# Optimization experiments

Hardware: AMD Instinct MI355X
Metric: run time of the kernel (lower is better)

Reference implementation:

```python
import jax, jax.numpy as jnp
import numpy as np

EPS = 1e-5

def _layernorm(x, g, b):
    m = jnp.mean(x, axis=-1, keepdims=True)
    v = jnp.mean((x - m) ** 2, axis=-1, keepdims=True)
    return (x - m) * jax.lax.rsqrt(v + EPS) * g + b

def setup_inputs() -> dict:
    key = jax.random.key(0)
    ks = jax.random.split(key, 16)
    B, N, L, E, D, NL = 1, 40962, 256, 4, 163848, 6
    inp = {}
    inp['mesh_latent'] = jax.random.normal(ks[0], (B, N, L), dtype=jnp.float32)
    inp['edge_index'] = jax.random.randint(ks[1], (2, D), 0, N, dtype=jnp.int32)
    inp['edge_attr'] = jax.random.normal(ks[2], (D, E), dtype=jnp.float32)
    s_e = 1.0 / np.sqrt(2 * L + E)
    s_n = 1.0 / np.sqrt(2 * L)
    s_o = 1.0 / np.sqrt(L)
    inp['We_w'] = jax.random.uniform(ks[3], (NL, 2 * L + E, L), jnp.float32, -s_e, s_e)
    inp['We_b'] = jax.random.uniform(ks[4], (NL, L), jnp.float32, -s_e, s_e)
    inp['ln1_g'] = jnp.ones((NL, L), jnp.float32)
    inp['ln1_b'] = jnp.zeros((NL, L), jnp.float32)
    inp['Wn1_w'] = jax.random.uniform(ks[5], (NL, 2 * L, L), jnp.float32, -s_n, s_n)
    inp['Wn1_b'] = jax.random.uniform(ks[6], (NL, L), jnp.float32, -s_n, s_n)
    inp['ln2_g'] = jnp.ones((NL, L), jnp.float32)
    inp['ln2_b'] = jnp.zeros((NL, L), jnp.float32)
    inp['Wn2_w'] = jax.random.uniform(ks[7], (NL, L, L), jnp.float32, -s_o, s_o)
    inp['Wn2_b'] = jax.random.uniform(ks[8], (NL, L), jnp.float32, -s_o, s_o)
    return inp

def reference(mesh_latent, edge_index, edge_attr, We_w, We_b, ln1_g, ln1_b,
              Wn1_w, Wn1_b, ln2_g, ln2_b, Wn2_w, Wn2_b):
    src = edge_index[0]  # x_j (source)
    dst = edge_index[1]  # x_i (target), also aggregation index
    N = mesh_latent.shape[1]
    L = mesh_latent.shape[2]
    # precompute edge_attr contribution is layer-dependent, done inside scan

    def layer(x, p):
        we_w, we_b, g1, b1, wn1_w, wn1_b, g2, b2, wn2_w, wn2_b = p
        x_i = x[dst]  # [E, L] target node feats
        x_j = x[src]  # [E, L] source node feats
        # edge MLP on cat([x_i, x_j, edge_attr]) without materializing the concat
        h = x_i @ we_w[:L] + x_j @ we_w[L:2 * L] + edge_attr @ we_w[2 * L:] + we_b
        msg = jax.nn.silu(_layernorm(h, g1, b1))  # [E, L]
        agg = jax.ops.segment_sum(msg, dst, num_segments=N)  # [N, L]
        u = x @ wn1_w[:L] + agg @ wn1_w[L:] + wn1_b
        u = jax.nn.silu(_layernorm(u, g2, b2)) @ wn2_w + wn2_b
        return x + u, None

    params = (We_w, We_b, ln1_g, ln1_b, Wn1_w, Wn1_b, ln2_g, ln2_b, Wn2_w, Wn2_b)

    def per_sample(x):
        x_out, _ = jax.lax.scan(layer, x, params)
        return x_out

    return jax.vmap(per_sample)(mesh_latent)
```

## Files before the change

### kernel.cpp

```cpp
#include <hip/hip_runtime.h>
#include <hip/hip_bf16.h>
#include <math.h>


#define NNODES 40962
#define NEDGES 163848
#define NLAYERS 6

typedef __attribute__((ext_vector_type(8))) short short8;
typedef __attribute__((ext_vector_type(4))) float f32x4;

__device__ __forceinline__ void async_copy16(void* lds, const void* g) {
    __builtin_amdgcn_global_load_lds(
        (const __attribute__((address_space(1))) unsigned int*)g,
        (__attribute__((address_space(3))) unsigned int*)lds, 16, 0, 0);
}

__global__ __launch_bounds__(256) void wprep_kernel(
    const float* __restrict__ src, unsigned short* __restrict__ dst,
    int R, int C, size_t src_lstride, size_t src_hstride, int halves)
{
    __shared__ float t[32][33];
    const int b = blockIdx.z;
    src += (size_t)(b / halves) * src_lstride + (size_t)(b % halves) * src_hstride;
    dst += (size_t)b * R * C;
    const int tx = threadIdx.x & 31, ty = threadIdx.x >> 5;
    const int c0 = blockIdx.x * 32, r0 = blockIdx.y * 32;
    #pragma unroll
    for (int i = 0; i < 4; ++i)
        t[ty + 8 * i][tx] = src[(size_t)(r0 + ty + 8 * i) * C + c0 + tx];
    __syncthreads();
    #pragma unroll
    for (int i = 0; i < 4; ++i) {
        unsigned int u = __float_as_uint(t[tx][ty + 8 * i]);
        unsigned short h = (unsigned short)((u + 0x7FFFu + ((u >> 16) & 1u)) >> 16);
        dst[(size_t)(c0 + ty + 8 * i) * R + r0 + tx] = h;
    }
}

__global__ __launch_bounds__(256) void gemm_mfma(
    const float* __restrict__ A1, const float* __restrict__ A2,
    const unsigned short* __restrict__ BT,
    const float* __restrict__ bias, const float* __restrict__ resid,
    float* __restrict__ C, int M, int K, int ldC)
{
    __shared__ __align__(16) short Ah[128 * 40];
    __shared__ __align__(16) short Al[128 * 40];
    __shared__ __align__(16) short Bs[128 * 32];

    const int tid = threadIdx.x;
    const int wave = tid >> 6;
    const int lane = tid & 63;
    const int m0 = blockIdx.x * 128;
    const int n0 = blockIdx.y * 128;
    const int wm = wave >> 1;
    const int wn = wave & 1;
    const int fm = lane & 15;
    const int quad = lane >> 4;
    const int ko = quad * 8;

    const int arow = tid >> 1;
    const int akh = (tid & 1) * 16;
    const int gr_stage = m0 + arow;

    f32x4 acc[4][4];
    #pragma unroll
    for (int i = 0; i < 4; ++i)
        #pragma unroll
        for (int j = 0; j < 4; ++j)
            acc[i][j] = (f32x4){0.f, 0.f, 0.f, 0.f};

    const int nkt = K >> 5;
    for (int kt = 0; kt < nkt; ++kt) {
        const int k0 = kt << 5;
        const float* Asrc; int kb;
        if (A2 != nullptr && k0 >= 256) { Asrc = A2; kb = k0 - 256; }
        else                            { Asrc = A1; kb = k0; }

        {
            const int n_row = wave * 32 + (lane >> 2);
            const char* gbase = (const char*)BT + (((size_t)(n0 + n_row) * K + k0) << 1)
                              + ((lane & 3) << 4);
            char* lbase = (char*)Bs + wave * 2048;
            async_copy16(lbase, gbase);
            const char* gbase2 = gbase + ((size_t)16 * K << 1);
            async_copy16(lbase + 1024, gbase2);
        }

        {
            float f[16];
            if (gr_stage < M) {
                const float* ap = Asrc + (size_t)gr_stage * 256 + kb + akh;
                #pragma unroll
                for (int i = 0; i < 4; ++i) {
                    f32x4 v = *(const f32x4*)(ap + 4 * i);
                    f[4 * i + 0] = v.x; f[4 * i + 1] = v.y;
                    f[4 * i + 2] = v.z; f[4 * i + 3] = v.w;
                }
            } else {
                #pragma unroll
                for (int i = 0; i < 16; ++i) f[i] = 0.f;
            }
            unsigned int hid[8], lod[8];
            #pragma unroll
            for (int i = 0; i < 8; ++i) {
                unsigned int u0 = __float_as_uint(f[2 * i]);
                unsigned int u1 = __float_as_uint(f[2 * i + 1]);
                float l0 = f[2 * i]     - __uint_as_float(u0 & 0xFFFF0000u);
                float l1 = f[2 * i + 1] - __uint_as_float(u1 & 0xFFFF0000u);
                hid[i] = (u0 >> 16) | (u1 & 0xFFFF0000u);
                lod[i] = (__float_as_uint(l0) >> 16) | (__float_as_uint(l1) & 0xFFFF0000u);
            }
            short* ah = &Ah[arow * 40 + akh];
            short* al = &Al[arow * 40 + akh];
            ((uint4*)ah)[0] = make_uint4(hid[0], hid[1], hid[2], hid[3]);
            ((uint4*)ah)[1] = make_uint4(hid[4], hid[5], hid[6], hid[7]);
            ((uint4*)al)[0] = make_uint4(lod[0], lod[1], lod[2], lod[3]);
            ((uint4*)al)[1] = make_uint4(lod[4], lod[5], lod[6], lod[7]);
        }

        __syncthreads();

        short8 afh[4], afl[4], bf[4];
        #pragma unroll
        for (int i = 0; i < 4; ++i) {
            const int r = wm * 64 + i * 16 + fm;
            afh[i] = *(const short8*)&Ah[r * 40 + ko];
            afl[i] = *(const short8*)&Al[r * 40 + ko];
        }
        #pragma unroll
        for (int j = 0; j < 4; ++j) {
            const int r = wn * 64 + j * 16 + fm;
            bf[j] = *(const short8*)&Bs[r * 32 + ko];
        }
        #pragma unroll
        for (int i = 0; i < 4; ++i)
            #pragma unroll
            for (int j = 0; j < 4; ++j) {
                acc[i][j] = __builtin_amdgcn_mfma_f32_16x16x32_bf16(afl[i], bf[j], acc[i][j], 0, 0, 0);
                acc[i][j] = __builtin_amdgcn_mfma_f32_16x16x32_bf16(afh[i], bf[j], acc[i][j], 0, 0, 0);
            }

        __syncthreads();
    }

    #pragma unroll
    for (int j = 0; j < 4; ++j) {
        const int gc = n0 + wn * 64 + j * 16 + fm;
        const float bj = bias ? bias[gc] : 0.f;
        #pragma unroll
        for (int i = 0; i < 4; ++i) {
            #pragma unroll
            for (int r = 0; r < 4; ++r) {
                const int gr = m0 + wm * 64 + i * 16 + quad * 4 + r;
                if (gr < M) {
                    float v = acc[i][j][r] + bj;
                    if (resid) v += resid[(size_t)gr * ldC + gc];
                    C[(size_t)gr * ldC + gc] = v;
                }
            }
        }
    }
}

__device__ __forceinline__ float wave_sum(float v) {
    #pragma unroll
    for (int o = 32; o > 0; o >>= 1) v += __shfl_xor(v, o);
    return v;
}

__global__ __launch_bounds__(256) void count_kernel(
    const int* __restrict__ dst, int* __restrict__ deg, int E)
{
    int e = blockIdx.x * 256 + threadIdx.x;
    if (e < E) atomicAdd(&deg[dst[e]], 1);
}

__global__ __launch_bounds__(1024) void scan_kernel(
    const int* __restrict__ deg, int* __restrict__ rowptr, int n)
{
    __shared__ int wsum[16];
    __shared__ int carry_s;
    const int tid = threadIdx.x;
    const int lane = tid & 63, wave = tid >> 6;
    if (tid == 0) carry_s = 0;
    __syncthreads();

    for (int base = 0; base < n; base += 1024) {
        int i = base + tid;
        int v = (i < n) ? deg[i] : 0;
        int x = v;
        #pragma unroll
        for (int o = 1; o < 64; o <<= 1) {
            int t = __shfl_up(x, o);
            if (lane >= o) x += t;
        }
        if (lane == 63) wsum[wave] = x;
        __syncthreads();
        if (wave == 0 && lane < 16) {
            int w = wsum[lane];
            #pragma unroll
            for (int o = 1; o < 16; o <<= 1) {
                int t = __shfl_up(w, o);
                if (lane >= o) w += t;
            }
            wsum[lane] = w;
        }
        __syncthreads();
        int wave_off = (wave == 0) ? 0 : wsum[wave - 1];
        int incl = x + wave_off + carry_s;
        if (i < n) rowptr[i] = incl - v;
        __syncthreads();
        if (tid == 0) carry_s += wsum[15];
        __syncthreads();
    }
    if (tid == 0) rowptr[n] = carry_s;
}

__global__ __launch_bounds__(256) void scatter_kernel(
    const int* __restrict__ dst, int* __restrict__ cursor,
    int* __restrict__ esorted, int E)
{
    int e = blockIdx.x * 256 + threadIdx.x;
    if (e < E) {
        int p = atomicAdd(&cursor[dst[e]], 1);
        esorted[p] = e;
    }
}

__global__ __launch_bounds__(256) void node_agg_kernel(
    const float* __restrict__ P,
    const int* __restrict__ src,
    const float* __restrict__ attr,
    const float* __restrict__ W3,
    const float* __restrict__ be, const float* __restrict__ g1, const float* __restrict__ b1,
    const int* __restrict__ rowptr, const int* __restrict__ esorted,
    float* __restrict__ agg, int N)
{
    const int wave = threadIdx.x >> 6;
    const int lane = threadIdx.x & 63;
    const int n = blockIdx.x * 4 + wave;
    if (n >= N) return;
    const int c0 = lane * 4;

    float4 p1 = *(const float4*)(P + (size_t)n * 512 + c0);
    const float* p1p = (const float*)&p1;

    float w30[4], w31[4], w32[4], w33[4], bev[4], g1v[4], b1v[4];
    #pragma unroll
    for (int i = 0; i < 4; ++i) {
        const int c = c0 + i;
        w30[i] = W3[c]; w31[i] = W3[256 + c]; w32[i] = W3[512 + c]; w33[i] = W3[768 + c];
        bev[i] = be[c]; g1v[i] = g1[c]; b1v[i] = b1[c];
    }

    float acc[4] = {0.f, 0.f, 0.f, 0.f};
    const int beg = rowptr[n];
    const int end = rowptr[n + 1];

    for (int i = beg; i < end; ++i) {
        const int e = esorted[i];
        const int s = src[e];
        float4 ps = *(const float4*)(P + (size_t)s * 512 + 256 + c0);
        const float* psp = (const float*)&ps;
        float4 av = *(const float4*)(attr + (size_t)e * 4);

        float h[4];
        #pragma unroll
        for (int j = 0; j < 4; ++j) {
            float w = av.x * w30[j] + av.y * w31[j] + av.z * w32[j] + av.w * w33[j];
            h[j] = p1p[j] + psp[j] + w + bev[j];
        }

        float sum = wave_sum(h[0] + h[1] + h[2] + h[3]);
        const float mean = sum * (1.0f / 256.0f);
        float vs = 0.f;
        #pragma unroll
        for (int j = 0; j < 4; ++j) { float t = h[j] - mean; vs += t * t; }
        vs = wave_sum(vs);
        const float rstd = rsqrtf(vs * (1.0f / 256.0f) + 1e-5f);

        #pragma unroll
        for (int j = 0; j < 4; ++j) {
            float y = (h[j] - mean) * rstd * g1v[j] + b1v[j];
            acc[j] += y / (1.0f + __expf(-y));
        }
    }

    *(float4*)(agg + (size_t)n * 256 + c0) = make_float4(acc[0], acc[1], acc[2], acc[3]);
}

__global__ __launch_bounds__(256) void ln_silu_kernel(
    float* __restrict__ u, const float* __restrict__ g, const float* __restrict__ b, int N)
{
    const int wave = threadIdx.x >> 6;
    const int lane = threadIdx.x & 63;
    const int r = blockIdx.x * 4 + wave;
    if (r >= N) return;

    float4 hv = *(const float4*)(u + (size_t)r * 256 + lane * 4);
    float h[4] = {hv.x, hv.y, hv.z, hv.w};

    float sum = wave_sum(h[0] + h[1] + h[2] + h[3]);
    const float mean = sum * (1.0f / 256.0f);
    float vs = 0.f;
    #pragma unroll
    for (int i = 0; i < 4; ++i) { float t = h[i] - mean; vs += t * t; }
    vs = wave_sum(vs);
    const float rstd = rsqrtf(vs * (1.0f / 256.0f) + 1e-5f);

    #pragma unroll
    for (int i = 0; i < 4; ++i) {
        const int c = lane * 4 + i;
        float y = (h[i] - mean) * rstd * g[c] + b[c];
        h[i] = y / (1.0f + __expf(-y));
    }
    *(float4*)(u + (size_t)r * 256 + lane * 4) = make_float4(h[0], h[1], h[2], h[3]);
}

extern "C" void kernel_launch(void* const* d_in, const int* in_sizes, int n_in,
                              void* d_out, int out_size, void* d_ws, size_t ws_size,
                              hipStream_t stream) {
    const float* mesh   = (const float*)d_in[0];
    const int*   eidx   = (const int*)  d_in[1];
    const float* eattr  = (const float*)d_in[2];
    const float* We_w   = (const float*)d_in[3];
    const float* We_b   = (const float*)d_in[4];
    const float* ln1_g  = (const float*)d_in[5];
    const float* ln1_b  = (const float*)d_in[6];
    const float* Wn1_w  = (const float*)d_in[7];
    const float* Wn1_b  = (const float*)d_in[8];
    const float* ln2_g  = (const float*)d_in[9];
    const float* ln2_b  = (const float*)d_in[10];
    const float* Wn2_w  = (const float*)d_in[11];
    const float* Wn2_b  = (const float*)d_in[12];

    const int N = NNODES, E = NEDGES;

    float* x   = (float*)d_out;
    float* P   = (float*)d_ws;
    float* u   = P;
    float* agg = P + (size_t)N * 512;
    int*   deg     = (int*)(agg + (size_t)N * 256);
    int*   rowptr  = deg + N;
    int*   cursor  = rowptr + (N + 1);
    int*   esorted = cursor + N;
    uintptr_t wp = (uintptr_t)(esorted + E);
    wp = (wp + 63) & ~(uintptr_t)63;
    unsigned short* BTe  = (unsigned short*)wp;
    unsigned short* BTn1 = BTe  + (size_t)6 * 512 * 256;
    unsigned short* BTn2 = BTn1 + (size_t)6 * 256 * 512;

    const int* src = eidx;
    const int* dst = eidx + E;

    hipMemcpyAsync(x, mesh, (size_t)N * 256 * sizeof(float),
                   hipMemcpyDeviceToDevice, stream);

    wprep_kernel<<<dim3(8, 8, 12), 256, 0, stream>>>(
        We_w, BTe, 256, 256, (size_t)516 * 256, (size_t)256 * 256, 2);
    wprep_kernel<<<dim3(8, 16, 6), 256, 0, stream>>>(
        Wn1_w, BTn1, 512, 256, (size_t)512 * 256, 0, 1);
    wprep_kernel<<<dim3(8, 8, 6), 256, 0, stream>>>(
        Wn2_w, BTn2, 256, 256, (size_t)256 * 256, 0, 1);

    hipMemsetAsync(deg, 0, (size_t)N * sizeof(int), stream);
    count_kernel<<<(E + 255) / 256, 256, 0, stream>>>(dst, deg, E);
    scan_kernel<<<1, 1024, 0, stream>>>(deg, rowptr, N);
    hipMemcpyAsync(cursor, rowptr, (size_t)N * sizeof(int),
                   hipMemcpyDeviceToDevice, stream);
    scatter_kernel<<<(E + 255) / 256, 256, 0, stream>>>(dst, cursor, esorted, E);

    const int mblocks = (N + 127) / 128;
    const int node_blocks = (N + 3) / 4;

    for (int l = 0; l < NLAYERS; ++l) {
        const float* W3  = We_w + (size_t)l * 516 * 256 + (size_t)512 * 256;
        const float* be  = We_b  + (size_t)l * 256;
        const float* g1  = ln1_g + (size_t)l * 256;
        const float* b1  = ln1_b + (size_t)l * 256;
        const float* bn1 = Wn1_b + (size_t)l * 256;
        const float* g2  = ln2_g + (size_t)l * 256;
        const float* b2  = ln2_b + (size_t)l * 256;
        const float* bn2 = Wn2_b + (size_t)l * 256;
        const unsigned short* bte  = BTe  + (size_t)l * 512 * 256;
        const unsigned short* btn1 = BTn1 + (size_t)l * 256 * 512;
        const unsigned short* btn2 = BTn2 + (size_t)l * 256 * 256;

        gemm_mfma<<<dim3(mblocks, 4), 256, 0, stream>>>(
            x, nullptr, bte, nullptr, nullptr, P, N, 256, 512);
        node_agg_kernel<<<node_blocks, 256, 0, stream>>>(
            P, src, eattr, W3, be, g1, b1, rowptr, esorted, agg, N);
        gemm_mfma<<<dim3(mblocks, 2), 256, 0, stream>>>(
            x, agg, btn1, bn1, nullptr, u, N, 512, 256);
        ln_silu_kernel<<<node_blocks, 256, 0, stream>>>(u, g2, b2, N);
        gemm_mfma<<<dim3(mblocks, 2), 256, 0, stream>>>(
            u, nullptr, btn2, bn2, x, x, N, 256, 256);
    }
}
```

Baseline: 1.527 ms.

## Fuse node LayerNorm+SiLU into GEMM A-load and prefetch edges in aggregation

The ln_silu kernel is replaced by a stats-only kernel that writes per-row mean and rstd. The LayerNorm and SiLU are then applied while the third GEMM stages its A tile, which removes one full read-modify-write pass over u. The node aggregation loop now prefetches the next edge's gather and attribute loads, and it computes mean and variance in a single fused shuffle reduction (E[x^2]-mean^2). The single-pass variance is less numerically robust, and the GEMM load path gains extra per-element exp work.

```diff
diff --git a/kernel.cpp b/kernel.cpp
--- a/kernel.cpp
+++ b/kernel.cpp
@@ -42,6 +42,8 @@
     const float* __restrict__ A1, const float* __restrict__ A2,
     const unsigned short* __restrict__ BT,
     const float* __restrict__ bias, const float* __restrict__ resid,
+    const float2* __restrict__ lnstats, const float* __restrict__ lng,
+    const float* __restrict__ lnb,
     float* __restrict__ C, int M, int K, int ldC)
 {
     __shared__ __align__(16) short Ah[128 * 40];
@@ -96,6 +98,15 @@
                     f32x4 v = *(const f32x4*)(ap + 4 * i);
                     f[4 * i + 0] = v.x; f[4 * i + 1] = v.y;
                     f[4 * i + 2] = v.z; f[4 * i + 3] = v.w;
+                }
+                if (lnstats != nullptr) {
+                    const float2 st = lnstats[gr_stage];
+                    #pragma unroll
+                    for (int i = 0; i < 16; ++i) {
+                        const int c = k0 + akh + i;
+                        float y = (f[i] - st.x) * st.y * lng[c] + lnb[c];
+                        f[i] = y / (1.0f + __expf(-y));
+                    }
                 }
             } else {
                 #pragma unroll
@@ -258,27 +269,43 @@
     const int beg = rowptr[n];
     const int end = rowptr[n + 1];
 
+    float4 ps = make_float4(0.f, 0.f, 0.f, 0.f);
+    float4 av = make_float4(0.f, 0.f, 0.f, 0.f);
+    if (beg < end) {
+        const int e = esorted[beg];
+        const int s = src[e];
+        ps = *(const float4*)(P + (size_t)s * 512 + 256 + c0);
+        av = *(const float4*)(attr + (size_t)e * 4);
+    }
+
     for (int i = beg; i < end; ++i) {
-        const int e = esorted[i];
-        const int s = src[e];
-        float4 ps = *(const float4*)(P + (size_t)s * 512 + 256 + c0);
-        const float* psp = (const float*)&ps;
-        float4 av = *(const float4*)(attr + (size_t)e * 4);
-
+        const float4 ps_c = ps;
+        const float4 av_c = av;
+        if (i + 1 < end) {
+            const int e2 = esorted[i + 1];
+            const int s2 = src[e2];
+            ps = *(const float4*)(P + (size_t)s2 * 512 + 256 + c0);
+            av = *(const float4*)(attr + (size_t)e2 * 4);
+        }
+
+        const float* psp = (const float*)&ps_c;
         float h[4];
         #pragma unroll
         for (int j = 0; j < 4; ++j) {
-            float w = av.x * w30[j] + av.y * w31[j] + av.z * w32[j] + av.w * w33[j];
+            float w = av_c.x * w30[j] + av_c.y * w31[j] + av_c.z * w32[j] + av_c.w * w33[j];
             h[j] = p1p[j] + psp[j] + w + bev[j];
         }
 
-        float sum = wave_sum(h[0] + h[1] + h[2] + h[3]);
-        const float mean = sum * (1.0f / 256.0f);
-        float vs = 0.f;
-        #pragma unroll
-        for (int j = 0; j < 4; ++j) { float t = h[j] - mean; vs += t * t; }
-        vs = wave_sum(vs);
-        const float rstd = rsqrtf(vs * (1.0f / 256.0f) + 1e-5f);
+        float s_ = h[0] + h[1] + h[2] + h[3];
+        float q_ = h[0] * h[0] + h[1] * h[1] + h[2] * h[2] + h[3] * h[3];
+        #pragma unroll
+        for (int o = 32; o > 0; o >>= 1) {
+            s_ += __shfl_xor(s_, o);
+            q_ += __shfl_xor(q_, o);
+        }
+        const float mean = s_ * (1.0f / 256.0f);
+        const float var  = q_ * (1.0f / 256.0f) - mean * mean;
+        const float rstd = rsqrtf(var + 1e-5f);
 
         #pragma unroll
         for (int j = 0; j < 4; ++j) {
@@ -290,8 +317,8 @@
     *(float4*)(agg + (size_t)n * 256 + c0) = make_float4(acc[0], acc[1], acc[2], acc[3]);
 }
 
-__global__ __launch_bounds__(256) void ln_silu_kernel(
-    float* __restrict__ u, const float* __restrict__ g, const float* __restrict__ b, int N)
+__global__ __launch_bounds__(256) void row_stats_kernel(
+    const float* __restrict__ u, float2* __restrict__ stats, int N)
 {
     const int wave = threadIdx.x >> 6;
     const int lane = threadIdx.x & 63;
@@ -299,23 +326,18 @@
     if (r >= N) return;
 
     float4 hv = *(const float4*)(u + (size_t)r * 256 + lane * 4);
-    float h[4] = {hv.x, hv.y, hv.z, hv.w};
-
-    float sum = wave_sum(h[0] + h[1] + h[2] + h[3]);
-    const float mean = sum * (1.0f / 256.0f);
-    float vs = 0.f;
-    #pragma unroll
-    for (int i = 0; i < 4; ++i) { float t = h[i] - mean; vs += t * t; }
-    vs = wave_sum(vs);
-    const float rstd = rsqrtf(vs * (1.0f / 256.0f) + 1e-5f);
-
-    #pragma unroll
-    for (int i = 0; i < 4; ++i) {
-        const int c = lane * 4 + i;
-        float y = (h[i] - mean) * rstd * g[c] + b[c];
-        h[i] = y / (1.0f + __expf(-y));
-    }
-    *(float4*)(u + (size_t)r * 256 + lane * 4) = make_float4(h[0], h[1], h[2], h[3]);
+    float s_ = hv.x + hv.y + hv.z + hv.w;
+    float q_ = hv.x * hv.x + hv.y * hv.y + hv.z * hv.z + hv.w * hv.w;
+    #pragma unroll
+    for (int o = 32; o > 0; o >>= 1) {
+        s_ += __shfl_xor(s_, o);
+        q_ += __shfl_xor(q_, o);
+    }
+    if (lane == 0) {
+        const float mean = s_ * (1.0f / 256.0f);
+        const float var  = q_ * (1.0f / 256.0f) - mean * mean;
+        stats[r] = make_float2(mean, rsqrtf(var + 1e-5f));
+    }
 }
 
 extern "C" void kernel_launch(void* const* d_in, const int* in_sizes, int n_in,
@@ -350,6 +372,7 @@
     unsigned short* BTe  = (unsigned short*)wp;
     unsigned short* BTn1 = BTe  + (size_t)6 * 512 * 256;
     unsigned short* BTn2 = BTn1 + (size_t)6 * 256 * 512;
+    float2* stats = (float2*)(BTn2 + (size_t)6 * 256 * 256);
 
     const int* src = eidx;
     const int* dst = eidx + E;
@@ -388,13 +411,16 @@
         const unsigned short* btn2 = BTn2 + (size_t)l * 256 * 256;
 
         gemm_mfma<<<dim3(mblocks, 4), 256, 0, stream>>>(
-            x, nullptr, bte, nullptr, nullptr, P, N, 256, 512);
+            x, nullptr, bte, nullptr, nullptr, nullptr, nullptr, nullptr,
+            P, N, 256, 512);
         node_agg_kernel<<<node_blocks, 256, 0, stream>>>(
             P, src, eattr, W3, be, g1, b1, rowptr, esorted, agg, N);
         gemm_mfma<<<dim3(mblocks, 2), 256, 0, stream>>>(
-            x, agg, btn1, bn1, nullptr, u, N, 512, 256);
-        ln_silu_kernel<<<node_blocks, 256, 0, stream>>>(u, g2, b2, N);
+            x, agg, btn1, bn1, nullptr, nullptr, nullptr, nullptr,
+            u, N, 512, 256);
+        row_stats_kernel<<<node_blocks, 256, 0, stream>>>(u, stats, N);
         gemm_mfma<<<dim3(mblocks, 2), 256, 0, stream>>>(
-            u, nullptr, btn2, bn2, x, x, N, 256, 256);
-    }
-}
+            u, nullptr, btn2, bn2, x, stats, g2, b2,
+            x, N, 256, 256);
+    }
+}
```

After: 1.588 ms. 4.0% more time.

## Store activations pre-split into bf16 hi/lo planes and async-load GEMM A tiles

Applied to the files above, without the earlier changes.

Producers now write activations as separate bf16 high and low planes: the init copy, the node aggregation, the LN+SiLU kernel and the residual GEMM epilogue. The GEMM can then stage its A tiles straight into LDS with global_load_lds instead of loading fp32, splitting in registers and storing. This halves A-operand bytes per GEMM and removes the split ALU work from the inner loop. In exchange it adds extra hi/lo stores in the epilogues and drops the LDS padding, which may cause bank conflicts. The node aggregation kernel also processes two edges per wave using 32-lane halves with 8 columns each, and both layernorms switch to a single-pass sum and sum-of-squares variance.

```diff
diff --git a/kernel.cpp b/kernel.cpp
--- a/kernel.cpp
+++ b/kernel.cpp
@@ -14,6 +14,14 @@
     __builtin_amdgcn_global_load_lds(
         (const __attribute__((address_space(1))) unsigned int*)g,
         (__attribute__((address_space(3))) unsigned int*)lds, 16, 0, 0);
+}
+
+__device__ __forceinline__ void split2(float a, float b, unsigned int& hi, unsigned int& lo) {
+    unsigned int u0 = __float_as_uint(a), u1 = __float_as_uint(b);
+    float l0 = a - __uint_as_float(u0 & 0xFFFF0000u);
+    float l1 = b - __uint_as_float(u1 & 0xFFFF0000u);
+    hi = (u0 >> 16) | (u1 & 0xFFFF0000u);
+    lo = (__float_as_uint(l0) >> 16) | (__float_as_uint(l1) & 0xFFFF0000u);
 }
 
 __global__ __launch_bounds__(256) void wprep_kernel(
@@ -38,30 +46,41 @@
     }
 }
 
+__global__ __launch_bounds__(256) void init_split_kernel(
+    const float* __restrict__ mesh, float* __restrict__ x,
+    unsigned short* __restrict__ xh, unsigned short* __restrict__ xl, int total4)
+{
+    int i = blockIdx.x * 256 + threadIdx.x;
+    if (i >= total4) return;
+    f32x4 v = ((const f32x4*)mesh)[i];
+    ((f32x4*)x)[i] = v;
+    unsigned int h0, l0, h1, l1;
+    split2(v.x, v.y, h0, l0);
+    split2(v.z, v.w, h1, l1);
+    ((uint2*)xh)[i] = make_uint2(h0, h1);
+    ((uint2*)xl)[i] = make_uint2(l0, l1);
+}
+
 __global__ __launch_bounds__(256) void gemm_mfma(
-    const float* __restrict__ A1, const float* __restrict__ A2,
+    const unsigned short* __restrict__ A1h, const unsigned short* __restrict__ A1l,
+    const unsigned short* __restrict__ A2h, const unsigned short* __restrict__ A2l,
     const unsigned short* __restrict__ BT,
     const float* __restrict__ bias, const float* __restrict__ resid,
-    float* __restrict__ C, int M, int K, int ldC)
-{
-    __shared__ __align__(16) short Ah[128 * 40];
-    __shared__ __align__(16) short Al[128 * 40];
+    float* __restrict__ C, unsigned short* __restrict__ Ch, unsigned short* __restrict__ Cl,
+    int M, int K, int ldC)
+{
+    __shared__ __align__(16) short Ah[128 * 32];
+    __shared__ __align__(16) short Al[128 * 32];
     __shared__ __align__(16) short Bs[128 * 32];
 
     const int tid = threadIdx.x;
-    const int wave = tid >> 6;
-    const int lane = tid & 63;
-    const int m0 = blockIdx.x * 128;
-    const int n0 = blockIdx.y * 128;
-    const int wm = wave >> 1;
-    const int wn = wave & 1;
-    const int fm = lane & 15;
-    const int quad = lane >> 4;
-    const int ko = quad * 8;
-
-    const int arow = tid >> 1;
-    const int akh = (tid & 1) * 16;
-    const int gr_stage = m0 + arow;
+    const int wave = tid >> 6, lane = tid & 63;
+    const int m0 = blockIdx.x * 128, n0 = blockIdx.y * 128;
+    const int wm = wave >> 1, wn = wave & 1;
+    const int fm = lane & 15, quad = lane >> 4, ko = quad * 8;
+
+    const int r_in = lane >> 2;
+    const int seg  = lane & 3;
 
     f32x4 acc[4][4];
     #pragma unroll
@@ -73,50 +92,18 @@
     const int nkt = K >> 5;
     for (int kt = 0; kt < nkt; ++kt) {
         const int k0 = kt << 5;
-        const float* Asrc; int kb;
-        if (A2 != nullptr && k0 >= 256) { Asrc = A2; kb = k0 - 256; }
-        else                            { Asrc = A1; kb = k0; }
-
-        {
-            const int n_row = wave * 32 + (lane >> 2);
-            const char* gbase = (const char*)BT + (((size_t)(n0 + n_row) * K + k0) << 1)
-                              + ((lane & 3) << 4);
-            char* lbase = (char*)Bs + wave * 2048;
-            async_copy16(lbase, gbase);
-            const char* gbase2 = gbase + ((size_t)16 * K << 1);
-            async_copy16(lbase + 1024, gbase2);
-        }
-
-        {
-            float f[16];
-            if (gr_stage < M) {
-                const float* ap = Asrc + (size_t)gr_stage * 256 + kb + akh;
-                #pragma unroll
-                for (int i = 0; i < 4; ++i) {
-                    f32x4 v = *(const f32x4*)(ap + 4 * i);
-                    f[4 * i + 0] = v.x; f[4 * i + 1] = v.y;
-                    f[4 * i + 2] = v.z; f[4 * i + 3] = v.w;
-                }
-            } else {
-                #pragma unroll
-                for (int i = 0; i < 16; ++i) f[i] = 0.f;
-            }
-            unsigned int hid[8], lod[8];
-            #pragma unroll
-            for (int i = 0; i < 8; ++i) {
-                unsigned int u0 = __float_as_uint(f[2 * i]);
-                unsigned int u1 = __float_as_uint(f[2 * i + 1]);
-                float l0 = f[2 * i]     - __uint_as_float(u0 & 0xFFFF0000u);
-                float l1 = f[2 * i + 1] - __uint_as_float(u1 & 0xFFFF0000u);
-                hid[i] = (u0 >> 16) | (u1 & 0xFFFF0000u);
-                lod[i] = (__float_as_uint(l0) >> 16) | (__float_as_uint(l1) & 0xFFFF0000u);
-            }
-            short* ah = &Ah[arow * 40 + akh];
-            short* al = &Al[arow * 40 + akh];
-            ((uint4*)ah)[0] = make_uint4(hid[0], hid[1], hid[2], hid[3]);
-            ((uint4*)ah)[1] = make_uint4(hid[4], hid[5], hid[6], hid[7]);
-            ((uint4*)al)[0] = make_uint4(lod[0], lod[1], lod[2], lod[3]);
-            ((uint4*)al)[1] = make_uint4(lod[4], lod[5], lod[6], lod[7]);
+        const unsigned short *Ahs, *Als; int kb;
+        if (A2h != nullptr && k0 >= 256) { Ahs = A2h; Als = A2l; kb = k0 - 256; }
+        else                             { Ahs = A1h; Als = A1l; kb = k0; }
+
+        #pragma unroll
+        for (int i = 0; i < 2; ++i) {
+            const int r = wave * 32 + i * 16 + r_in;
+            int gr = m0 + r; if (gr > M - 1) gr = M - 1;
+            const int lbase = (wave * 32 + i * 16) * 32;
+            async_copy16(&Ah[lbase], Ahs + (size_t)gr * 256 + kb + seg * 8);
+            async_copy16(&Al[lbase], Als + (size_t)gr * 256 + kb + seg * 8);
+            async_copy16(&Bs[lbase], BT + (size_t)(n0 + r) * K + k0 + seg * 8);
         }
 
         __syncthreads();
@@ -125,8 +112,8 @@
         #pragma unroll
         for (int i = 0; i < 4; ++i) {
             const int r = wm * 64 + i * 16 + fm;
-            afh[i] = *(const short8*)&Ah[r * 40 + ko];
-            afl[i] = *(const short8*)&Al[r * 40 + ko];
+            afh[i] = *(const short8*)&Ah[r * 32 + ko];
+            afl[i] = *(const short8*)&Al[r * 32 + ko];
         }
         #pragma unroll
         for (int j = 0; j < 4; ++j) {
@@ -157,16 +144,16 @@
                     float v = acc[i][j][r] + bj;
                     if (resid) v += resid[(size_t)gr * ldC + gc];
                     C[(size_t)gr * ldC + gc] = v;
+                    if (Ch) {
+                        unsigned int u = __float_as_uint(v);
+                        float lo = v - __uint_as_float(u & 0xFFFF0000u);
+                        Ch[(size_t)gr * ldC + gc] = (unsigned short)(u >> 16);
+                        Cl[(size_t)gr * ldC + gc] = (unsigned short)(__float_as_uint(lo) >> 16);
+                    }
                 }
             }
         }
     }
-}
-
-__device__ __forceinline__ float wave_sum(float v) {
-    #pragma unroll
-    for (int o = 32; o > 0; o >>= 1) v += __shfl_xor(v, o);
-    return v;
 }
 
 __global__ __launch_bounds__(256) void count_kernel(
@@ -235,63 +222,97 @@
     const float* __restrict__ W3,
     const float* __restrict__ be, const float* __restrict__ g1, const float* __restrict__ b1,
     const int* __restrict__ rowptr, const int* __restrict__ esorted,
-    float* __restrict__ agg, int N)
+    unsigned short* __restrict__ aggh, unsigned short* __restrict__ aggl, int N)
 {
     const int wave = threadIdx.x >> 6;
     const int lane = threadIdx.x & 63;
+    const int half = lane >> 5;
+    const int l32  = lane & 31;
     const int n = blockIdx.x * 4 + wave;
     if (n >= N) return;
-    const int c0 = lane * 4;
-
-    float4 p1 = *(const float4*)(P + (size_t)n * 512 + c0);
-    const float* p1p = (const float*)&p1;
-
-    float w30[4], w31[4], w32[4], w33[4], bev[4], g1v[4], b1v[4];
-    #pragma unroll
-    for (int i = 0; i < 4; ++i) {
-        const int c = c0 + i;
-        w30[i] = W3[c]; w31[i] = W3[256 + c]; w32[i] = W3[512 + c]; w33[i] = W3[768 + c];
-        bev[i] = be[c]; g1v[i] = g1[c]; b1v[i] = b1[c];
-    }
-
-    float acc[4] = {0.f, 0.f, 0.f, 0.f};
+    const int c0 = l32 * 8;
+
+    float p1[8];
+    {
+        f32x4 a = *(const f32x4*)(P + (size_t)n * 512 + c0);
+        f32x4 b = *(const f32x4*)(P + (size_t)n * 512 + c0 + 4);
+        p1[0] = a.x; p1[1] = a.y; p1[2] = a.z; p1[3] = a.w;
+        p1[4] = b.x; p1[5] = b.y; p1[6] = b.z; p1[7] = b.w;
+    }
+
+    float w3v[4][8], bev[8], g1v[8], b1v[8];
+    #pragma unroll
+    for (int r = 0; r < 4; ++r) {
+        f32x4 a = *(const f32x4*)(W3 + r * 256 + c0);
+        f32x4 b = *(const f32x4*)(W3 + r * 256 + c0 + 4);
+        w3v[r][0] = a.x; w3v[r][1] = a.y; w3v[r][2] = a.z; w3v[r][3] = a.w;
+        w3v[r][4] = b.x; w3v[r][5] = b.y; w3v[r][6] = b.z; w3v[r][7] = b.w;
+    }
+    {
+        f32x4 a, b;
+        a = *(const f32x4*)(be + c0); b = *(const f32x4*)(be + c0 + 4);
+        bev[0]=a.x; bev[1]=a.y; bev[2]=a.z; bev[3]=a.w; bev[4]=b.x; bev[5]=b.y; bev[6]=b.z; bev[7]=b.w;
+        a = *(const f32x4*)(g1 + c0); b = *(const f32x4*)(g1 + c0 + 4);
+        g1v[0]=a.x; g1v[1]=a.y; g1v[2]=a.z; g1v[3]=a.w; g1v[4]=b.x; g1v[5]=b.y; g1v[6]=b.z; g1v[7]=b.w;
+        a = *(const f32x4*)(b1 + c0); b = *(const f32x4*)(b1 + c0 + 4);
+        b1v[0]=a.x; b1v[1]=a.y; b1v[2]=a.z; b1v[3]=a.w; b1v[4]=b.x; b1v[5]=b.y; b1v[6]=b.z; b1v[7]=b.w;
+    }
+
+    float acc[8] = {0.f, 0.f, 0.f, 0.f, 0.f, 0.f, 0.f, 0.f};
     const int beg = rowptr[n];
     const int end = rowptr[n + 1];
 
-    for (int i = beg; i < end; ++i) {
+    for (int i = beg + half; i < end; i += 2) {
         const int e = esorted[i];
         const int s = src[e];
-        float4 ps = *(const float4*)(P + (size_t)s * 512 + 256 + c0);
-        const float* psp = (const float*)&ps;
-        float4 av = *(const float4*)(attr + (size_t)e * 4);
-
-        float h[4];
-        #pragma unroll
-        for (int j = 0; j < 4; ++j) {
-            float w = av.x * w30[j] + av.y * w31[j] + av.z * w32[j] + av.w * w33[j];
-            h[j] = p1p[j] + psp[j] + w + bev[j];
-        }
-
-        float sum = wave_sum(h[0] + h[1] + h[2] + h[3]);
-        const float mean = sum * (1.0f / 256.0f);
-        float vs = 0.f;
-        #pragma unroll
-        for (int j = 0; j < 4; ++j) { float t = h[j] - mean; vs += t * t; }
-        vs = wave_sum(vs);
-        const float rstd = rsqrtf(vs * (1.0f / 256.0f) + 1e-5f);
-
-        #pragma unroll
-        for (int j = 0; j < 4; ++j) {
+        f32x4 pa = *(const f32x4*)(P + (size_t)s * 512 + 256 + c0);
+        f32x4 pb = *(const f32x4*)(P + (size_t)s * 512 + 256 + c0 + 4);
+        f32x4 av = *(const f32x4*)(attr + (size_t)e * 4);
+        float ps[8] = {pa.x, pa.y, pa.z, pa.w, pb.x, pb.y, pb.z, pb.w};
+
+        float h[8];
+        #pragma unroll
+        for (int j = 0; j < 8; ++j) {
+            float w = av.x * w3v[0][j] + av.y * w3v[1][j] + av.z * w3v[2][j] + av.w * w3v[3][j];
+            h[j] = p1[j] + ps[j] + w + bev[j];
+        }
+
+        float s_ = ((h[0] + h[1]) + (h[2] + h[3])) + ((h[4] + h[5]) + (h[6] + h[7]));
+        float q_ = ((h[0]*h[0] + h[1]*h[1]) + (h[2]*h[2] + h[3]*h[3]))
+                 + ((h[4]*h[4] + h[5]*h[5]) + (h[6]*h[6] + h[7]*h[7]));
+        #pragma unroll
+        for (int o = 16; o > 0; o >>= 1) {
+            s_ += __shfl_xor(s_, o);
+            q_ += __shfl_xor(q_, o);
+        }
+        const float mean = s_ * (1.0f / 256.0f);
+        const float var  = q_ * (1.0f / 256.0f) - mean * mean;
+        const float rstd = rsqrtf(var + 1e-5f);
+
+        #pragma unroll
+        for (int j = 0; j < 8; ++j) {
             float y = (h[j] - mean) * rstd * g1v[j] + b1v[j];
             acc[j] += y / (1.0f + __expf(-y));
         }
     }
 
-    *(float4*)(agg + (size_t)n * 256 + c0) = make_float4(acc[0], acc[1], acc[2], acc[3]);
-}
-
-__global__ __launch_bounds__(256) void ln_silu_kernel(
-    float* __restrict__ u, const float* __restrict__ g, const float* __restrict__ b, int N)
+    #pragma unroll
+    for (int j = 0; j < 8; ++j) acc[j] += __shfl_xor(acc[j], 32);
+
+    if (half == 0) {
+        unsigned int h0, l0, h1, l1, h2, l2, h3, l3;
+        split2(acc[0], acc[1], h0, l0);
+        split2(acc[2], acc[3], h1, l1);
+        split2(acc[4], acc[5], h2, l2);
+        split2(acc[6], acc[7], h3, l3);
+        *(uint4*)(aggh + (size_t)n * 256 + c0) = make_uint4(h0, h1, h2, h3);
+        *(uint4*)(aggl + (size_t)n * 256 + c0) = make_uint4(l0, l1, l2, l3);
+    }
+}
+
+__global__ __launch_bounds__(256) void ln_silu_split_kernel(
+    const float* __restrict__ u, const float* __restrict__ g, const float* __restrict__ b,
+    unsigned short* __restrict__ uh, unsigned short* __restrict__ ul, int N)
 {
     const int wave = threadIdx.x >> 6;
     const int lane = threadIdx.x & 63;
@@ -301,13 +322,16 @@
     float4 hv = *(const float4*)(u + (size_t)r * 256 + lane * 4);
     float h[4] = {hv.x, hv.y, hv.z, hv.w};
 
-    float sum = wave_sum(h[0] + h[1] + h[2] + h[3]);
-    const float mean = sum * (1.0f / 256.0f);
-    float vs = 0.f;
-    #pragma unroll
-    for (int i = 0; i < 4; ++i) { float t = h[i] - mean; vs += t * t; }
-    vs = wave_sum(vs);
-    const float rstd = rsqrtf(vs * (1.0f / 256.0f) + 1e-5f);
+    float s_ = (h[0] + h[1]) + (h[2] + h[3]);
+    float q_ = (h[0]*h[0] + h[1]*h[1]) + (h[2]*h[2] + h[3]*h[3]);
+    #pragma unroll
+    for (int o = 32; o > 0; o >>= 1) {
+        s_ += __shfl_xor(s_, o);
+        q_ += __shfl_xor(q_, o);
+    }
+    const float mean = s_ * (1.0f / 256.0f);
+    const float var  = q_ * (1.0f / 256.0f) - mean * mean;
+    const float rstd = rsqrtf(var + 1e-5f);
 
     #pragma unroll
     for (int i = 0; i < 4; ++i) {
@@ -315,7 +339,11 @@
         float y = (h[i] - mean) * rstd * g[c] + b[c];
         h[i] = y / (1.0f + __expf(-y));
     }
-    *(float4*)(u + (size_t)r * 256 + lane * 4) = make_float4(h[0], h[1], h[2], h[3]);
+    unsigned int h0, l0, h1, l1;
+    split2(h[0], h[1], h0, l0);
+    split2(h[2], h[3], h1, l1);
+    ((uint2*)(uh + (size_t)r * 256))[lane] = make_uint2(h0, h1);
+    ((uint2*)(ul + (size_t)r * 256))[lane] = make_uint2(l0, l1);
 }
 
 extern "C" void kernel_launch(void* const* d_in, const int* in_sizes, int n_in,
@@ -337,14 +365,21 @@
 
     const int N = NNODES, E = NEDGES;
 
-    float* x   = (float*)d_out;
-    float* P   = (float*)d_ws;
-    float* u   = P;
-    float* agg = P + (size_t)N * 512;
-    int*   deg     = (int*)(agg + (size_t)N * 256);
-    int*   rowptr  = deg + N;
-    int*   cursor  = rowptr + (N + 1);
-    int*   esorted = cursor + N;
+    float* x = (float*)d_out;
+
+    float* P = (float*)d_ws;
+    float* u = P;
+    unsigned short* uh = (unsigned short*)(P + (size_t)N * 256);
+    unsigned short* ul = uh + (size_t)N * 256;
+
+    unsigned short* xh   = (unsigned short*)(P + (size_t)N * 512);
+    unsigned short* xl   = xh + (size_t)N * 256;
+    unsigned short* aggh = xl + (size_t)N * 256;
+    unsigned short* aggl = aggh + (size_t)N * 256;
+    int* deg     = (int*)(aggl + (size_t)N * 256);
+    int* rowptr  = deg + N;
+    int* cursor  = rowptr + (N + 1);
+    int* esorted = cursor + N;
     uintptr_t wp = (uintptr_t)(esorted + E);
     wp = (wp + 63) & ~(uintptr_t)63;
     unsigned short* BTe  = (unsigned short*)wp;
@@ -354,8 +389,8 @@
     const int* src = eidx;
     const int* dst = eidx + E;
 
-    hipMemcpyAsync(x, mesh, (size_t)N * 256 * sizeof(float),
-                   hipMemcpyDeviceToDevice, stream);
+    const int total4 = N * 64;
+    init_split_kernel<<<(total4 + 255) / 256, 256, 0, stream>>>(mesh, x, xh, xl, total4);
 
     wprep_kernel<<<dim3(8, 8, 12), 256, 0, stream>>>(
         We_w, BTe, 256, 256, (size_t)516 * 256, (size_t)256 * 256, 2);
@@ -388,13 +423,16 @@
         const unsigned short* btn2 = BTn2 + (size_t)l * 256 * 256;
 
         gemm_mfma<<<dim3(mblocks, 4), 256, 0, stream>>>(
-            x, nullptr, bte, nullptr, nullptr, P, N, 256, 512);
+            xh, xl, nullptr, nullptr, bte, nullptr, nullptr,
+            P, nullptr, nullptr, N, 256, 512);
         node_agg_kernel<<<node_blocks, 256, 0, stream>>>(
-            P, src, eattr, W3, be, g1, b1, rowptr, esorted, agg, N);
+            P, src, eattr, W3, be, g1, b1, rowptr, esorted, aggh, aggl, N);
         gemm_mfma<<<dim3(mblocks, 2), 256, 0, stream>>>(
-            x, agg, btn1, bn1, nullptr, u, N, 512, 256);
-        ln_silu_kernel<<<node_blocks, 256, 0, stream>>>(u, g2, b2, N);
+            xh, xl, aggh, aggl, btn1, bn1, nullptr,
+            u, nullptr, nullptr, N, 512, 256);
+        ln_silu_split_kernel<<<node_blocks, 256, 0, stream>>>(u, g2, b2, uh, ul, N);
         gemm_mfma<<<dim3(mblocks, 2), 256, 0, stream>>>(
-            u, nullptr, btn2, bn2, x, x, N, 256, 256);
-    }
-}
+            uh, ul, nullptr, nullptr, btn2, bn2, x,
+            x, xh, xl, N, 256, 256);
+    }
+}
```

Result: slower. 1.738 ms (+13.8%).

## Drop LDS staging in GEMM and fuse LayerNorm+SiLU into Wn2 GEMM prologue

Applied to the files above, without the earlier changes.

The GEMM kernel no longer stages A and B tiles through shared memory with barriers. Each wave now loads its MFMA fragments straight from global memory and splits fp32 A into hi/lo bf16 in registers. The separate LN2+SiLU pass is replaced by a row-statistics kernel that writes only mean/rstd. The final GEMM applies normalization and SiLU to A on load, which saves a full read-modify-write of u. The cost is redundant global loads, since each A row is reloaded by both wn waves and each B row by both wm waves, with no coalesced LDS reuse; the SiLU is also recomputed per N-tile. The variance now uses E[x^2]-mean^2, which is less numerically stable.

```diff
diff --git a/kernel.cpp b/kernel.cpp
--- a/kernel.cpp
+++ b/kernel.cpp
@@ -10,10 +10,23 @@
 typedef __attribute__((ext_vector_type(8))) short short8;
 typedef __attribute__((ext_vector_type(4))) float f32x4;
 
-__device__ __forceinline__ void async_copy16(void* lds, const void* g) {
-    __builtin_amdgcn_global_load_lds(
-        (const __attribute__((address_space(1))) unsigned int*)g,
-        (__attribute__((address_space(3))) unsigned int*)lds, 16, 0, 0);
+union pack8 { uint4 u4; short8 s8; };
+
+__device__ __forceinline__ void split8(const float* f, short8& hi, short8& lo) {
+    unsigned int h[4], l[4];
+    #pragma unroll
+    for (int i = 0; i < 4; ++i) {
+        unsigned int u0 = __float_as_uint(f[2 * i]);
+        unsigned int u1 = __float_as_uint(f[2 * i + 1]);
+        float l0 = f[2 * i]     - __uint_as_float(u0 & 0xFFFF0000u);
+        float l1 = f[2 * i + 1] - __uint_as_float(u1 & 0xFFFF0000u);
+        h[i] = (u0 >> 16) | (u1 & 0xFFFF0000u);
+        l[i] = (__float_as_uint(l0) >> 16) | (__float_as_uint(l1) & 0xFFFF0000u);
+    }
+    pack8 ph, pl;
+    ph.u4 = make_uint4(h[0], h[1], h[2], h[3]);
+    pl.u4 = make_uint4(l[0], l[1], l[2], l[3]);
+    hi = ph.s8; lo = pl.s8;
 }
 
 __global__ __launch_bounds__(256) void wprep_kernel(
@@ -42,26 +55,28 @@
     const float* __restrict__ A1, const float* __restrict__ A2,
     const unsigned short* __restrict__ BT,
     const float* __restrict__ bias, const float* __restrict__ resid,
+    const float2* __restrict__ lnstats, const float* __restrict__ lng,
+    const float* __restrict__ lnb,
     float* __restrict__ C, int M, int K, int ldC)
 {
-    __shared__ __align__(16) short Ah[128 * 40];
-    __shared__ __align__(16) short Al[128 * 40];
-    __shared__ __align__(16) short Bs[128 * 32];
-
     const int tid = threadIdx.x;
-    const int wave = tid >> 6;
-    const int lane = tid & 63;
-    const int m0 = blockIdx.x * 128;
-    const int n0 = blockIdx.y * 128;
-    const int wm = wave >> 1;
-    const int wn = wave & 1;
-    const int fm = lane & 15;
-    const int quad = lane >> 4;
-    const int ko = quad * 8;
-
-    const int arow = tid >> 1;
-    const int akh = (tid & 1) * 16;
-    const int gr_stage = m0 + arow;
+    const int wave = tid >> 6, lane = tid & 63;
+    const int m0 = blockIdx.x * 128, n0 = blockIdx.y * 128;
+    const int wm = wave >> 1, wn = wave & 1;
+    const int fm = lane & 15, quad = lane >> 4, ko = quad * 8;
+
+    int arow[4];
+    float2 st[4];
+    #pragma unroll
+    for (int i = 0; i < 4; ++i) {
+        int r = m0 + wm * 64 + i * 16 + fm;
+        arow[i] = (r < M) ? r : (M - 1);
+        st[i] = lnstats ? lnstats[arow[i]] : make_float2(0.f, 0.f);
+    }
+    const unsigned short* brow[4];
+    #pragma unroll
+    for (int j = 0; j < 4; ++j)
+        brow[j] = BT + (size_t)(n0 + wn * 64 + j * 16 + fm) * K;
 
     f32x4 acc[4][4];
     #pragma unroll
@@ -77,62 +92,40 @@
         if (A2 != nullptr && k0 >= 256) { Asrc = A2; kb = k0 - 256; }
         else                            { Asrc = A1; kb = k0; }
 
-        {
-            const int n_row = wave * 32 + (lane >> 2);
-            const char* gbase = (const char*)BT + (((size_t)(n0 + n_row) * K + k0) << 1)
-                              + ((lane & 3) << 4);
-            char* lbase = (char*)Bs + wave * 2048;
-            async_copy16(lbase, gbase);
-            const char* gbase2 = gbase + ((size_t)16 * K << 1);
-            async_copy16(lbase + 1024, gbase2);
-        }
-
-        {
-            float f[16];
-            if (gr_stage < M) {
-                const float* ap = Asrc + (size_t)gr_stage * 256 + kb + akh;
+        short8 bf[4];
+        #pragma unroll
+        for (int j = 0; j < 4; ++j)
+            bf[j] = *(const short8*)(brow[j] + k0 + ko);
+
+        float gg[8], bb[8];
+        if (lnstats) {
+            f32x4 g0 = *(const f32x4*)(lng + k0 + ko);
+            f32x4 g1 = *(const f32x4*)(lng + k0 + ko + 4);
+            f32x4 b0 = *(const f32x4*)(lnb + k0 + ko);
+            f32x4 b1 = *(const f32x4*)(lnb + k0 + ko + 4);
+            gg[0]=g0.x; gg[1]=g0.y; gg[2]=g0.z; gg[3]=g0.w;
+            gg[4]=g1.x; gg[5]=g1.y; gg[6]=g1.z; gg[7]=g1.w;
+            bb[0]=b0.x; bb[1]=b0.y; bb[2]=b0.z; bb[3]=b0.w;
+            bb[4]=b1.x; bb[5]=b1.y; bb[6]=b1.z; bb[7]=b1.w;
+        }
+
+        short8 afh[4], afl[4];
+        #pragma unroll
+        for (int i = 0; i < 4; ++i) {
+            const float* ap = Asrc + (size_t)arow[i] * 256 + kb + ko;
+            f32x4 v0 = *(const f32x4*)ap;
+            f32x4 v1 = *(const f32x4*)(ap + 4);
+            float f[8] = {v0.x, v0.y, v0.z, v0.w, v1.x, v1.y, v1.z, v1.w};
+            if (lnstats) {
                 #pragma unroll
-                for (int i = 0; i < 4; ++i) {
-                    f32x4 v = *(const f32x4*)(ap + 4 * i);
-                    f[4 * i + 0] = v.x; f[4 * i + 1] = v.y;
-                    f[4 * i + 2] = v.z; f[4 * i + 3] = v.w;
+                for (int t = 0; t < 8; ++t) {
+                    float y = (f[t] - st[i].x) * st[i].y * gg[t] + bb[t];
+                    f[t] = y / (1.0f + __expf(-y));
                 }
-            } else {
-                #pragma unroll
-                for (int i = 0; i < 16; ++i) f[i] = 0.f;
             }
-            unsigned int hid[8], lod[8];
-            #pragma unroll
-            for (int i = 0; i < 8; ++i) {
-                unsigned int u0 = __float_as_uint(f[2 * i]);
-                unsigned int u1 = __float_as_uint(f[2 * i + 1]);
-                float l0 = f[2 * i]     - __uint_as_float(u0 & 0xFFFF0000u);
-                float l1 = f[2 * i + 1] - __uint_as_float(u1 & 0xFFFF0000u);
-                hid[i] = (u0 >> 16) | (u1 & 0xFFFF0000u);
-                lod[i] = (__float_as_uint(l0) >> 16) | (__float_as_uint(l1) & 0xFFFF0000u);
-            }
-            short* ah = &Ah[arow * 40 + akh];
-            short* al = &Al[arow * 40 + akh];
-            ((uint4*)ah)[0] = make_uint4(hid[0], hid[1], hid[2], hid[3]);
-            ((uint4*)ah)[1] = make_uint4(hid[4], hid[5], hid[6], hid[7]);
-            ((uint4*)al)[0] = make_uint4(lod[0], lod[1], lod[2], lod[3]);
-            ((uint4*)al)[1] = make_uint4(lod[4], lod[5], lod[6], lod[7]);
-        }
-
-        __syncthreads();
-
-        short8 afh[4], afl[4], bf[4];
-        #pragma unroll
-        for (int i = 0; i < 4; ++i) {
-            const int r = wm * 64 + i * 16 + fm;
-            afh[i] = *(const short8*)&Ah[r * 40 + ko];
-            afl[i] = *(const short8*)&Al[r * 40 + ko];
-        }
-        #pragma unroll
-        for (int j = 0; j < 4; ++j) {
-            const int r = wn * 64 + j * 16 + fm;
-            bf[j] = *(const short8*)&Bs[r * 32 + ko];
-        }
+            split8(f, afh[i], afl[i]);
+        }
+
         #pragma unroll
         for (int i = 0; i < 4; ++i)
             #pragma unroll
@@ -140,8 +133,6 @@
                 acc[i][j] = __builtin_amdgcn_mfma_f32_16x16x32_bf16(afl[i], bf[j], acc[i][j], 0, 0, 0);
                 acc[i][j] = __builtin_amdgcn_mfma_f32_16x16x32_bf16(afh[i], bf[j], acc[i][j], 0, 0, 0);
             }
-
-        __syncthreads();
     }
 
     #pragma unroll
@@ -290,8 +281,8 @@
     *(float4*)(agg + (size_t)n * 256 + c0) = make_float4(acc[0], acc[1], acc[2], acc[3]);
 }
 
-__global__ __launch_bounds__(256) void ln_silu_kernel(
-    float* __restrict__ u, const float* __restrict__ g, const float* __restrict__ b, int N)
+__global__ __launch_bounds__(256) void row_stats_kernel(
+    const float* __restrict__ u, float2* __restrict__ stats, int N)
 {
     const int wave = threadIdx.x >> 6;
     const int lane = threadIdx.x & 63;
@@ -299,23 +290,18 @@
     if (r >= N) return;
 
     float4 hv = *(const float4*)(u + (size_t)r * 256 + lane * 4);
-    float h[4] = {hv.x, hv.y, hv.z, hv.w};
-
-    float sum = wave_sum(h[0] + h[1] + h[2] + h[3]);
-    const float mean = sum * (1.0f / 256.0f);
-    float vs = 0.f;
-    #pragma unroll
-    for (int i = 0; i < 4; ++i) { float t = h[i] - mean; vs += t * t; }
-    vs = wave_sum(vs);
-    const float rstd = rsqrtf(vs * (1.0f / 256.0f) + 1e-5f);
-
-    #pragma unroll
-    for (int i = 0; i < 4; ++i) {
-        const int c = lane * 4 + i;
-        float y = (h[i] - mean) * rstd * g[c] + b[c];
-        h[i] = y / (1.0f + __expf(-y));
-    }
-    *(float4*)(u + (size_t)r * 256 + lane * 4) = make_float4(h[0], h[1], h[2], h[3]);
+    float s_ = (hv.x + hv.y) + (hv.z + hv.w);
+    float q_ = (hv.x * hv.x + hv.y * hv.y) + (hv.z * hv.z + hv.w * hv.w);
+    #pragma unroll
+    for (int o = 32; o > 0; o >>= 1) {
+        s_ += __shfl_xor(s_, o);
+        q_ += __shfl_xor(q_, o);
+    }
+    if (lane == 0) {
+        const float mean = s_ * (1.0f / 256.0f);
+        const float var  = q_ * (1.0f / 256.0f) - mean * mean;
+        stats[r] = make_float2(mean, rsqrtf(var + 1e-5f));
+    }
 }
 
 extern "C" void kernel_launch(void* const* d_in, const int* in_sizes, int n_in,
@@ -350,6 +336,7 @@
     unsigned short* BTe  = (unsigned short*)wp;
     unsigned short* BTn1 = BTe  + (size_t)6 * 512 * 256;
     unsigned short* BTn2 = BTn1 + (size_t)6 * 256 * 512;
+    float2* stats = (float2*)(BTn2 + (size_t)6 * 256 * 256);
 
     const int* src = eidx;
     const int* dst = eidx + E;
@@ -388,13 +375,16 @@
         const unsigned short* btn2 = BTn2 + (size_t)l * 256 * 256;
 
         gemm_mfma<<<dim3(mblocks, 4), 256, 0, stream>>>(
-            x, nullptr, bte, nullptr, nullptr, P, N, 256, 512);
+            x, nullptr, bte, nullptr, nullptr, nullptr, nullptr, nullptr,
+            P, N, 256, 512);
         node_agg_kernel<<<node_blocks, 256, 0, stream>>>(
             P, src, eattr, W3, be, g1, b1, rowptr, esorted, agg, N);
         gemm_mfma<<<dim3(mblocks, 2), 256, 0, stream>>>(
-            x, agg, btn1, bn1, nullptr, u, N, 512, 256);
-        ln_silu_kernel<<<node_blocks, 256, 0, stream>>>(u, g2, b2, N);
+            x, agg, btn1, bn1, nullptr, nullptr, nullptr, nullptr,
+            u, N, 512, 256);
+        row_stats_kernel<<<node_blocks, 256, 0, stream>>>(u, stats, N);
         gemm_mfma<<<dim3(mblocks, 2), 256, 0, stream>>>(
-            u, nullptr, btn2, bn2, x, x, N, 256, 256);
-    }
-}
+            u, nullptr, btn2, bn2, x, stats, g2, b2,
+            x, N, 256, 256);
+    }
+}
```

Result: slower. 2.311 ms (+51.4%).
